# Kernel tuning notes

Hardware: AMD Instinct MI355X
Metric: run time of the kernel (lower is better)

The kernel has to match this reference:

```python
import jax, jax.numpy as jnp
import numpy as np

B, S, D = 2, 2048, 1024
H = 16
HEAD_DIM = 64          # matches head_dim init arg; D // H == 64
HALF_WINDOW = 32       # local_window_size // 2
SCALE = HEAD_DIM ** -0.5


def setup_inputs() -> dict:
    key = jax.random.key(0)
    ks = jax.random.split(key, 6)
    std = 1.0 / np.sqrt(D)
    return {
        "x": jax.random.normal(ks[0], (B, S, D), dtype=jnp.float32),
        "Wq": jax.random.normal(ks[1], (D, D), dtype=jnp.float32) * std,
        "Wk": jax.random.normal(ks[2], (D, D), dtype=jnp.float32) * std,
        "Wv": jax.random.normal(ks[3], (D, D), dtype=jnp.float32) * std,
        "Wo": jax.random.normal(ks[4], (D, D), dtype=jnp.float32) * std,
        "bo": jnp.zeros((D,), dtype=jnp.float32),
    }


def reference(x, Wq, Wk, Wv, Wo, bo):
    b, s, d = x.shape
    h, hd = H, d // H

    def split_heads(y):  # [b, s, d] -> [b, h, s, hd]
        return y.reshape(b, s, h, hd).transpose(0, 2, 1, 3)

    q = split_heads(x @ Wq) * SCALE
    k = split_heads(x @ Wk)
    v = split_heads(x @ Wv)

    # dense scores [b, h, s, s] (module materializes full O(S^2) matrix)
    scores = jnp.einsum("bhqd,bhkd->bhqk", q, k)

    # local window |i-j| <= HALF_WINDOW combined with causal j <= i
    i = jnp.arange(s)
    local = jnp.abs(i[:, None] - i[None, :]) <= HALF_WINDOW
    causal = i[None, :] <= i[:, None]
    mask = local & causal  # [s, s]
    scores = jnp.where(mask[None, None, :, :], scores, -jnp.inf)

    attn = jax.nn.softmax(scores, axis=-1)  # diagonal always valid -> no NaN
    out = jnp.einsum("bhqk,bhkd->bhqd", attn, v)
    out = out.transpose(0, 2, 1, 3).reshape(b, s, d)  # merge heads
    return out @ Wo + bo
```

## Files before the change

kernel.cpp:

```cpp
#include <hip/hip_runtime.h>
#include <hip/hip_bf16.h>

typedef __bf16 bf16_t;
typedef __bf16 bf16x8 __attribute__((ext_vector_type(8)));
typedef __bf16 bf16x4 __attribute__((ext_vector_type(4)));
typedef float  f32x4  __attribute__((ext_vector_type(4)));

#define B_   2
#define S_   2048
#define D_   1024
#define H_   16
#define HD_  64
#define HW   32
#define SCALE_ 0.125f

__device__ __forceinline__ void gl_lds16(const bf16_t* g, bf16_t* l) {
  __builtin_amdgcn_global_load_lds(
      (const __attribute__((address_space(1))) void*)g,
      (__attribute__((address_space(3))) void*)l, 16, 0, 0);
}

__global__ __launch_bounds__(256) void k_conv(const float* __restrict__ X,
                                              const float* __restrict__ W0,
                                              const float* __restrict__ W1,
                                              const float* __restrict__ W2,
                                              const float* __restrict__ W3,
                                              bf16_t* __restrict__ Xb,
                                              bf16_t* __restrict__ Wt) {
  __shared__ bf16_t t[64][72];
  int bid = blockIdx.x;
  int tid = threadIdx.x;
  if (bid < 2048) {
    int i = bid * 256 + tid;
    const float4 a = ((const float4*)X)[i * 2];
    const float4 b = ((const float4*)X)[i * 2 + 1];
    bf16x8 r;
    r[0] = (bf16_t)a.x; r[1] = (bf16_t)a.y; r[2] = (bf16_t)a.z; r[3] = (bf16_t)a.w;
    r[4] = (bf16_t)b.x; r[5] = (bf16_t)b.y; r[6] = (bf16_t)b.z; r[7] = (bf16_t)b.w;
    ((bf16x8*)Xb)[i] = r;
    return;
  }
  int wb = bid - 2048;
  int wsel = wb >> 8;
  const float* W = (wsel == 0) ? W0 : (wsel == 1) ? W1 : (wsel == 2) ? W2 : W3;
  bf16_t* dst = Wt + (size_t)wsel * D_ * D_;
  int tile = wb & 255;
  int k0 = (tile >> 4) * 64, n0 = (tile & 15) * 64;
  int r = tid >> 4, c4 = (tid & 15) * 4;
#pragma unroll
  for (int i = 0; i < 4; ++i) {
    int row = i * 16 + r;
    float4 v = *(const float4*)(W + (size_t)(k0 + row) * D_ + n0 + c4);
    t[row][c4 + 0] = (bf16_t)v.x;
    t[row][c4 + 1] = (bf16_t)v.y;
    t[row][c4 + 2] = (bf16_t)v.z;
    t[row][c4 + 3] = (bf16_t)v.w;
  }
  __syncthreads();
#pragma unroll
  for (int i = 0; i < 4; ++i) {
    int row = i * 16 + r;
    bf16x4 o;
    o[0] = t[c4 + 0][row];
    o[1] = t[c4 + 1][row];
    o[2] = t[c4 + 2][row];
    o[3] = t[c4 + 3][row];
    *(bf16x4*)(dst + (size_t)(n0 + row) * D_ + k0 + c4) = o;
  }
}

__global__ __launch_bounds__(256) void k_gemm_qkv(const bf16_t* __restrict__ X,
                                                  const bf16_t* __restrict__ Wt,
                                                  bf16_t* __restrict__ Q,
                                                  bf16_t* __restrict__ Kb,
                                                  bf16_t* __restrict__ V) {
  __shared__ bf16_t sA[3 * 128 * 32];
  __shared__ bf16_t sB[3 * 128 * 32];
  int bid = blockIdx.x;
  int mt = bid & 31, nt = bid >> 5;
  int wsel = nt >> 3;
  int n0 = (nt & 7) * 128, m0 = mt * 128;
  const bf16_t* Wp = Wt + (size_t)wsel * D_ * D_;
  int tid = threadIdx.x, lane = tid & 63, wave = tid >> 6;
  int wr = (wave >> 1) * 64, wc = (wave & 1) * 64;
  int r0 = wave * 32 + (lane >> 2);
  int ce = (((lane & 3) ^ ((lane >> 3) & 3))) * 8;
  const bf16_t* gA0 = X + (size_t)(m0 + r0) * D_ + ce;
  const bf16_t* gB0 = Wp + (size_t)(n0 + r0) * D_ + ce;
  int lofs = wave * 1024;
#define QSTAGE_(bi, kt) do { \
    gl_lds16(gA0 + (kt), sA + (bi) * 4096 + lofs);        \
    gl_lds16(gA0 + (kt) + (size_t)16 * D_, sA + (bi) * 4096 + lofs + 512); \
    gl_lds16(gB0 + (kt), sB + (bi) * 4096 + lofs);        \
    gl_lds16(gB0 + (kt) + (size_t)16 * D_, sB + (bi) * 4096 + lofs + 512); \
  } while (0)
  f32x4 acc[4][4] = {};
  int rl = lane & 15, hi = lane >> 4;
  int cofs = (hi ^ ((rl >> 1) & 3)) * 8;
  QSTAGE_(0, 0);
  QSTAGE_(1, 32);
  asm volatile("s_waitcnt vmcnt(4)" ::: "memory");
  __builtin_amdgcn_sched_barrier(0);
  __builtin_amdgcn_s_barrier();
  asm volatile("" ::: "memory");
  int cur = 0;
  for (int t = 0; t < 32; ++t) {
    const bf16_t* pA = sA + cur * 4096;
    const bf16_t* pB = sB + cur * 4096;
    bf16x8 af[4], bfr[4];
#pragma unroll
    for (int m = 0; m < 4; ++m)
      af[m] = *(const bf16x8*)&pA[(wr + m * 16 + rl) * 32 + cofs];
#pragma unroll
    for (int n = 0; n < 4; ++n)
      bfr[n] = *(const bf16x8*)&pB[(wc + n * 16 + rl) * 32 + cofs];
    int sb = cur + 2; if (sb >= 3) sb -= 3;
    if (t + 2 < 32) QSTAGE_(sb, (t + 2) * 32);
    __builtin_amdgcn_s_setprio(1);
#pragma unroll
    for (int m = 0; m < 4; ++m)
#pragma unroll
      for (int n = 0; n < 4; ++n)
        acc[m][n] = __builtin_amdgcn_mfma_f32_16x16x32_bf16(af[m], bfr[n], acc[m][n], 0, 0, 0);
    __builtin_amdgcn_s_setprio(0);
    if (t < 30) {
      asm volatile("s_waitcnt vmcnt(4)" ::: "memory");
    } else if (t == 30) {
      asm volatile("s_waitcnt vmcnt(0)" ::: "memory");
    }
    if (t < 31) {
      __builtin_amdgcn_sched_barrier(0);
      __builtin_amdgcn_s_barrier();
      asm volatile("" ::: "memory");
    }
    if (++cur == 3) cur = 0;
  }
#undef QSTAGE_
  if (wsel < 2) {
    float qscale = (wsel == 0) ? SCALE_ : 1.0f;
    bf16_t* Dst = wsel ? Kb : Q;
#pragma unroll
    for (int m = 0; m < 4; ++m) {
#pragma unroll
      for (int n = 0; n < 4; ++n) {
#pragma unroll
        for (int r = 0; r < 4; ++r) {
          int gm = m0 + wr + m * 16 + hi * 4 + r;
          int gn = n0 + wc + n * 16 + rl;
          int b = gm >> 11, s = gm & 2047;
          int h = gn >> 6, hd = gn & 63;
          Dst[(((size_t)(b * H_ + h)) * S_ + s) * HD_ + hd] = (bf16_t)(acc[m][n][r] * qscale);
        }
      }
    }
  } else {
    bf16_t* bounce = sA;
#pragma unroll
    for (int hh = 0; hh < 2; ++hh) {
      __syncthreads();
      if ((wave & 1) == hh) {
#pragma unroll
        for (int m = 0; m < 4; ++m)
#pragma unroll
          for (int n = 0; n < 4; ++n)
#pragma unroll
            for (int r = 0; r < 4; ++r)
              bounce[(n * 16 + rl) * 136 + wr + m * 16 + hi * 4 + r] = (bf16_t)acc[m][n][r];
      }
      __syncthreads();
#pragma unroll
      for (int ps = 0; ps < 4; ++ps) {
        int idx = ps * 256 + tid;
        int row = idx >> 4, c8 = (idx & 15) * 8;
        bf16x8 v = *(const bf16x8*)&bounce[row * 136 + c8];
        int gn = n0 + hh * 64 + row;
        int h = gn >> 6, hd = gn & 63;
        int gmS = m0 + c8;
        int b2 = gmS >> 11, s0 = gmS & 2047;
        *(bf16x8*)&V[(((size_t)(b2 * H_ + h)) * HD_ + hd) * S_ + s0] = v;
      }
    }
  }
}

__global__ __launch_bounds__(256) void k_gemm_out(const bf16_t* __restrict__ A,
                                                  const bf16_t* __restrict__ Wp,
                                                  const float* __restrict__ bo,
                                                  float* __restrict__ out) {
  __shared__ bf16_t sA[64 * 32];
  __shared__ bf16_t sB[128 * 32];
  int bid = blockIdx.x;
  int mt = bid & 63, nt = bid >> 6;
  int n0 = nt * 128, m0 = mt * 64;
  int tid = threadIdx.x, lane = tid & 63, wave = tid >> 6;
  int wc = wave * 32;
  int crow = lane >> 2, ccol = (lane & 3) * 8;
  const bf16_t* gsrc0; bf16_t* ldst0;
  const bf16_t* gsrc1; bf16_t* ldst1;
  const bf16_t* gsrc2; bf16_t* ldst2;
#pragma unroll
  for (int j = 0; j < 3; ++j) {
    int c = wave * 3 + j;
    const bf16_t* g; bf16_t* l;
    if (c < 4) {
      g = A + (size_t)(m0 + c * 16 + crow) * D_ + ccol;
      l = sA + c * 512;
    } else {
      g = Wp + (size_t)(n0 + (c - 4) * 16 + crow) * D_ + ccol;
      l = sB + (c - 4) * 512;
    }
    if (j == 0) { gsrc0 = g; ldst0 = l; }
    else if (j == 1) { gsrc1 = g; ldst1 = l; }
    else { gsrc2 = g; ldst2 = l; }
  }
  f32x4 acc[4][2] = {};
  int kq = (lane >> 4) * 8, rl = lane & 15, hi = lane >> 4;
  for (int kt = 0; kt < D_; kt += 32) {
    __syncthreads();
    gl_lds16(gsrc0 + kt, ldst0);
    gl_lds16(gsrc1 + kt, ldst1);
    gl_lds16(gsrc2 + kt, ldst2);
    __syncthreads();
    bf16x8 af[4], bfr[2];
#pragma unroll
    for (int m = 0; m < 4; ++m)
      af[m] = *(const bf16x8*)&sA[(m * 16 + rl) * 32 + kq];
#pragma unroll
    for (int n = 0; n < 2; ++n)
      bfr[n] = *(const bf16x8*)&sB[(wc + n * 16 + rl) * 32 + kq];
#pragma unroll
    for (int m = 0; m < 4; ++m)
#pragma unroll
      for (int n = 0; n < 2; ++n)
        acc[m][n] = __builtin_amdgcn_mfma_f32_16x16x32_bf16(af[m], bfr[n], acc[m][n], 0, 0, 0);
  }
#pragma unroll
  for (int m = 0; m < 4; ++m) {
#pragma unroll
    for (int n = 0; n < 2; ++n) {
#pragma unroll
      for (int r = 0; r < 4; ++r) {
        int gm = m0 + m * 16 + hi * 4 + r;
        int gn = n0 + wc + n * 16 + rl;
        out[(size_t)gm * D_ + gn] = acc[m][n][r] + bo[gn];
      }
    }
  }
}

#define QB 128
#define KW 160
#define VW 176
#define KLP 68
#define VTP 180

__global__ __launch_bounds__(256) void k_attn(const bf16_t* __restrict__ Q,
                                              const bf16_t* __restrict__ K,
                                              const bf16_t* __restrict__ Vt,
                                              bf16_t* __restrict__ O) {
  __shared__ bf16_t sK[KW][KLP];
  __shared__ bf16_t sV[HD_][VTP];
  __shared__ bf16_t sP[4][16][KLP];
  int bid = blockIdx.x;
  int qb = bid & 15, bh = bid >> 4;
  int q0 = qb * QB;
  const bf16_t* Kp = K + (size_t)bh * S_ * HD_;
  const bf16_t* Vp = Vt + (size_t)bh * HD_ * S_;
  const bf16_t* Qp = Q + (size_t)bh * S_ * HD_;
  int tid = threadIdx.x;
  int lane = tid & 63, wave = tid >> 6;
  int rl = lane & 15, hi = lane >> 4;
  int wk0b = q0 - HW;
  for (int idx = tid; idx < KW * 8; idx += 256) {
    int row = idx >> 3, c8 = (idx & 7) * 8;
    int kg = wk0b + row;
    kg = kg < 0 ? 0 : (kg > S_ - 1 ? S_ - 1 : kg);
    *(bf16x8*)&sK[row][c8] = *(const bf16x8*)(Kp + (size_t)kg * HD_ + c8);
  }
  for (int idx = tid; idx < HD_ * (VW / 8); idx += 256) {
    int row = idx / (VW / 8), c8 = (idx % (VW / 8)) * 8;
    int ks = wk0b + c8;
    ks = ks < 0 ? 0 : (ks > S_ - 8 ? S_ - 8 : ks);
    *(bf16x8*)&sV[row][c8] = *(const bf16x8*)(Vp + (size_t)row * S_ + ks);
  }
  __syncthreads();
  int b = bh >> 4, h = bh & 15;
#pragma unroll
  for (int qi = 0; qi < 2; ++qi) {
    int wko = qi * 64 + wave * 16;
    bf16x8 qf0 = *(const bf16x8*)(Qp + (size_t)(q0 + wko + rl) * HD_ + hi * 8);
    bf16x8 qf1 = *(const bf16x8*)(Qp + (size_t)(q0 + wko + rl) * HD_ + 32 + hi * 8);
    f32x4 accs[3] = {};
#pragma unroll
    for (int kb = 0; kb < 3; ++kb) {
      bf16x8 kf = *(const bf16x8*)&sK[wko + kb * 16 + rl][hi * 8];
      accs[kb] = __builtin_amdgcn_mfma_f32_16x16x32_bf16(kf, qf0, accs[kb], 0, 0, 0);
    }
#pragma unroll
    for (int kb = 0; kb < 3; ++kb) {
      bf16x8 kf = *(const bf16x8*)&sK[wko + kb * 16 + rl][32 + hi * 8];
      accs[kb] = __builtin_amdgcn_mfma_f32_16x16x32_bf16(kf, qf1, accs[kb], 0, 0, 0);
    }
    float p[3][4];
    float mx = -1e30f;
#pragma unroll
    for (int kb = 0; kb < 3; ++kb) {
#pragma unroll
      for (int r = 0; r < 4; ++r) {
        int kl = kb * 16 + hi * 4 + r;
        bool valid = (kl >= rl) && (kl <= rl + HW) && (wk0b + wko + kl >= 0);
        float s = valid ? accs[kb][r] : -1e30f;
        p[kb][r] = s;
        mx = fmaxf(mx, s);
      }
    }
    mx = fmaxf(mx, __shfl_xor(mx, 16));
    mx = fmaxf(mx, __shfl_xor(mx, 32));
    float sum = 0.f;
#pragma unroll
    for (int kb = 0; kb < 3; ++kb)
#pragma unroll
      for (int r = 0; r < 4; ++r) {
        p[kb][r] = __expf(p[kb][r] - mx);
        sum += p[kb][r];
      }
    sum += __shfl_xor(sum, 16);
    sum += __shfl_xor(sum, 32);
    float inv = 1.f / sum;
#pragma unroll
    for (int kb = 0; kb < 3; ++kb) {
      bf16x4 pv;
#pragma unroll
      for (int r = 0; r < 4; ++r) pv[r] = (bf16_t)(p[kb][r] * inv);
      *(bf16x4*)&sP[wave][rl][kb * 16 + hi * 4] = pv;
    }
    {
      bf16x4 z4;
#pragma unroll
      for (int r = 0; r < 4; ++r) z4[r] = (bf16_t)0.f;
      *(bf16x4*)&sP[wave][rl][48 + hi * 4] = z4;
    }
    f32x4 acco[4] = {};
#pragma unroll
    for (int ks = 0; ks < 2; ++ks) {
      bf16x8 aP = *(const bf16x8*)&sP[wave][rl][ks * 32 + hi * 8];
#pragma unroll
      for (int n = 0; n < 4; ++n) {
        bf16x8 bV = *(const bf16x8*)&sV[n * 16 + rl][wko + ks * 32 + hi * 8];
        acco[n] = __builtin_amdgcn_mfma_f32_16x16x32_bf16(aP, bV, acco[n], 0, 0, 0);
      }
    }
#pragma unroll
    for (int n = 0; n < 4; ++n) {
#pragma unroll
      for (int r = 0; r < 4; ++r) {
        int qgl = q0 + wko + hi * 4 + r;
        int d = n * 16 + rl;
        O[((size_t)(b * S_ + qgl)) * D_ + h * HD_ + d] = (bf16_t)acco[n][r];
      }
    }
  }
}

extern "C" void kernel_launch(void* const* d_in, const int* in_sizes, int n_in,
                              void* d_out, int out_size, void* d_ws, size_t ws_size,
                              hipStream_t stream) {
  const float* x  = (const float*)d_in[0];
  const float* Wq = (const float*)d_in[1];
  const float* Wk = (const float*)d_in[2];
  const float* Wv = (const float*)d_in[3];
  const float* Wo = (const float*)d_in[4];
  const float* bo = (const float*)d_in[5];
  float* out = (float*)d_out;
  char* ws = (char*)d_ws;
  bf16_t* xb = (bf16_t*)(ws);
  bf16_t* wt = (bf16_t*)(ws + (size_t)(8 << 20));
  bf16_t* qb = (bf16_t*)(ws + (size_t)(16 << 20));
  bf16_t* kb = (bf16_t*)(ws + (size_t)(24 << 20));
  bf16_t* vb = (bf16_t*)(ws + (size_t)(32 << 20));
  bf16_t* ob = (bf16_t*)(ws + (size_t)(40 << 20));

  hipLaunchKernelGGL(k_conv, dim3(3072), dim3(256), 0, stream,
                     x, Wq, Wk, Wv, Wo, xb, wt);
  hipLaunchKernelGGL(k_gemm_qkv, dim3(768), dim3(256), 0, stream, xb, wt, qb, kb, vb);
  hipLaunchKernelGGL(k_attn, dim3(512), dim3(256), 0, stream, qb, kb, vb, ob);
  hipLaunchKernelGGL(k_gemm_out, dim3(512), dim3(256), 0, stream,
                     ob, wt + (size_t)3 * D_ * D_, bo, out);
}
```

Before: 79.72 us.

## Fuse activation fp32-to-bf16 conversion into QKV GEMM A-tile loading

Drops the separate pass that converted x to bf16 in a workspace buffer; the conversion kernel now only transposes and converts the weights. The QKV GEMM reads fp32 x directly, holds the tile two steps ahead in registers, converts it to bf16, and writes it to LDS in the same swizzled layout the direct global-to-LDS loads used. This removes a full write and re-read of the bf16 activation copy and shrinks the conversion launch. In exchange the GEMM fetches twice as many bytes for A, spends registers and conversion instructions per K step, and adds an LDS-store wait before each barrier.

Measured after the change: 101.5 us. 1.27x slower.

```diff
diff --git a/kernel.cpp b/kernel.cpp
--- a/kernel.cpp
+++ b/kernel.cpp
@@ -20,31 +20,18 @@
       (__attribute__((address_space(3))) void*)l, 16, 0, 0);
 }
 
-__global__ __launch_bounds__(256) void k_conv(const float* __restrict__ X,
-                                              const float* __restrict__ W0,
-                                              const float* __restrict__ W1,
-                                              const float* __restrict__ W2,
-                                              const float* __restrict__ W3,
-                                              bf16_t* __restrict__ Xb,
-                                              bf16_t* __restrict__ Wt) {
+__global__ __launch_bounds__(256) void k_convw(const float* __restrict__ W0,
+                                               const float* __restrict__ W1,
+                                               const float* __restrict__ W2,
+                                               const float* __restrict__ W3,
+                                               bf16_t* __restrict__ Wt) {
   __shared__ bf16_t t[64][72];
   int bid = blockIdx.x;
   int tid = threadIdx.x;
-  if (bid < 2048) {
-    int i = bid * 256 + tid;
-    const float4 a = ((const float4*)X)[i * 2];
-    const float4 b = ((const float4*)X)[i * 2 + 1];
-    bf16x8 r;
-    r[0] = (bf16_t)a.x; r[1] = (bf16_t)a.y; r[2] = (bf16_t)a.z; r[3] = (bf16_t)a.w;
-    r[4] = (bf16_t)b.x; r[5] = (bf16_t)b.y; r[6] = (bf16_t)b.z; r[7] = (bf16_t)b.w;
-    ((bf16x8*)Xb)[i] = r;
-    return;
-  }
-  int wb = bid - 2048;
-  int wsel = wb >> 8;
+  int wsel = bid >> 8;
   const float* W = (wsel == 0) ? W0 : (wsel == 1) ? W1 : (wsel == 2) ? W2 : W3;
   bf16_t* dst = Wt + (size_t)wsel * D_ * D_;
-  int tile = wb & 255;
+  int tile = bid & 255;
   int k0 = (tile >> 4) * 64, n0 = (tile & 15) * 64;
   int r = tid >> 4, c4 = (tid & 15) * 4;
 #pragma unroll
@@ -69,7 +56,7 @@
   }
 }
 
-__global__ __launch_bounds__(256) void k_gemm_qkv(const bf16_t* __restrict__ X,
+__global__ __launch_bounds__(256) void k_gemm_qkv(const float* __restrict__ Xf,
                                                   const bf16_t* __restrict__ Wt,
                                                   bf16_t* __restrict__ Q,
                                                   bf16_t* __restrict__ Kb,
@@ -85,26 +72,61 @@
   int wr = (wave >> 1) * 64, wc = (wave & 1) * 64;
   int r0 = wave * 32 + (lane >> 2);
   int ce = (((lane & 3) ^ ((lane >> 3) & 3))) * 8;
-  const bf16_t* gA0 = X + (size_t)(m0 + r0) * D_ + ce;
-  const bf16_t* gB0 = Wp + (size_t)(n0 + r0) * D_ + ce;
+  const float*  gA0f = Xf + (size_t)(m0 + r0) * D_ + ce;
+  const bf16_t* gB0  = Wp + (size_t)(n0 + r0) * D_ + ce;
   int lofs = wave * 1024;
-#define QSTAGE_(bi, kt) do { \
-    gl_lds16(gA0 + (kt), sA + (bi) * 4096 + lofs);        \
-    gl_lds16(gA0 + (kt) + (size_t)16 * D_, sA + (bi) * 4096 + lofs + 512); \
-    gl_lds16(gB0 + (kt), sB + (bi) * 4096 + lofs);        \
-    gl_lds16(gB0 + (kt) + (size_t)16 * D_, sB + (bi) * 4096 + lofs + 512); \
-  } while (0)
+  int lane8 = lane * 8;
   f32x4 acc[4][4] = {};
   int rl = lane & 15, hi = lane >> 4;
   int cofs = (hi ^ ((rl >> 1) & 3)) * 8;
-  QSTAGE_(0, 0);
-  QSTAGE_(1, 32);
-  asm volatile("s_waitcnt vmcnt(4)" ::: "memory");
+  gl_lds16(gB0, sB + lofs);
+  gl_lds16(gB0 + (size_t)16 * D_, sB + lofs + 512);
+  {
+    float4 x0 = *(const float4*)(gA0f);
+    float4 x1 = *(const float4*)(gA0f + 4);
+    float4 x2 = *(const float4*)(gA0f + (size_t)16 * D_);
+    float4 x3 = *(const float4*)(gA0f + (size_t)16 * D_ + 4);
+    bf16x8 va, vb;
+    va[0] = (bf16_t)x0.x; va[1] = (bf16_t)x0.y; va[2] = (bf16_t)x0.z; va[3] = (bf16_t)x0.w;
+    va[4] = (bf16_t)x1.x; va[5] = (bf16_t)x1.y; va[6] = (bf16_t)x1.z; va[7] = (bf16_t)x1.w;
+    vb[0] = (bf16_t)x2.x; vb[1] = (bf16_t)x2.y; vb[2] = (bf16_t)x2.z; vb[3] = (bf16_t)x2.w;
+    vb[4] = (bf16_t)x3.x; vb[5] = (bf16_t)x3.y; vb[6] = (bf16_t)x3.z; vb[7] = (bf16_t)x3.w;
+    *(bf16x8*)(sA + lofs + lane8) = va;
+    *(bf16x8*)(sA + lofs + 512 + lane8) = vb;
+  }
+  float4 aR0 = *(const float4*)(gA0f + 32);
+  float4 aR1 = *(const float4*)(gA0f + 36);
+  float4 aR2 = *(const float4*)(gA0f + 32 + (size_t)16 * D_);
+  float4 aR3 = *(const float4*)(gA0f + 36 + (size_t)16 * D_);
+  gl_lds16(gB0 + 32, sB + 4096 + lofs);
+  gl_lds16(gB0 + 32 + (size_t)16 * D_, sB + 4096 + lofs + 512);
+  asm volatile("s_waitcnt vmcnt(6)" ::: "memory");
+  asm volatile("s_waitcnt lgkmcnt(0)" ::: "memory");
   __builtin_amdgcn_sched_barrier(0);
   __builtin_amdgcn_s_barrier();
   asm volatile("" ::: "memory");
   int cur = 0;
   for (int t = 0; t < 32; ++t) {
+    int wnext = cur + 1; if (wnext >= 3) wnext -= 3;
+    int sb = cur + 2; if (sb >= 3) sb -= 3;
+    if (t + 1 < 32) {
+      bf16x8 va, vb;
+      va[0] = (bf16_t)aR0.x; va[1] = (bf16_t)aR0.y; va[2] = (bf16_t)aR0.z; va[3] = (bf16_t)aR0.w;
+      va[4] = (bf16_t)aR1.x; va[5] = (bf16_t)aR1.y; va[6] = (bf16_t)aR1.z; va[7] = (bf16_t)aR1.w;
+      vb[0] = (bf16_t)aR2.x; vb[1] = (bf16_t)aR2.y; vb[2] = (bf16_t)aR2.z; vb[3] = (bf16_t)aR2.w;
+      vb[4] = (bf16_t)aR3.x; vb[5] = (bf16_t)aR3.y; vb[6] = (bf16_t)aR3.z; vb[7] = (bf16_t)aR3.w;
+      *(bf16x8*)(sA + wnext * 4096 + lofs + lane8) = va;
+      *(bf16x8*)(sA + wnext * 4096 + lofs + 512 + lane8) = vb;
+    }
+    if (t + 2 < 32) {
+      int kt2 = (t + 2) * 32;
+      aR0 = *(const float4*)(gA0f + kt2);
+      aR1 = *(const float4*)(gA0f + kt2 + 4);
+      aR2 = *(const float4*)(gA0f + kt2 + (size_t)16 * D_);
+      aR3 = *(const float4*)(gA0f + kt2 + (size_t)16 * D_ + 4);
+      gl_lds16(gB0 + kt2, sB + sb * 4096 + lofs);
+      gl_lds16(gB0 + kt2 + (size_t)16 * D_, sB + sb * 4096 + lofs + 512);
+    }
     const bf16_t* pA = sA + cur * 4096;
     const bf16_t* pB = sB + cur * 4096;
     bf16x8 af[4], bfr[4];
@@ -114,8 +136,6 @@
 #pragma unroll
     for (int n = 0; n < 4; ++n)
       bfr[n] = *(const bf16x8*)&pB[(wc + n * 16 + rl) * 32 + cofs];
-    int sb = cur + 2; if (sb >= 3) sb -= 3;
-    if (t + 2 < 32) QSTAGE_(sb, (t + 2) * 32);
     __builtin_amdgcn_s_setprio(1);
 #pragma unroll
     for (int m = 0; m < 4; ++m)
@@ -123,19 +143,19 @@
       for (int n = 0; n < 4; ++n)
         acc[m][n] = __builtin_amdgcn_mfma_f32_16x16x32_bf16(af[m], bfr[n], acc[m][n], 0, 0, 0);
     __builtin_amdgcn_s_setprio(0);
-    if (t < 30) {
-      asm volatile("s_waitcnt vmcnt(4)" ::: "memory");
+    if (t <= 29) {
+      asm volatile("s_waitcnt vmcnt(6)" ::: "memory");
     } else if (t == 30) {
       asm volatile("s_waitcnt vmcnt(0)" ::: "memory");
     }
+    asm volatile("s_waitcnt lgkmcnt(0)" ::: "memory");
     if (t < 31) {
       __builtin_amdgcn_sched_barrier(0);
       __builtin_amdgcn_s_barrier();
       asm volatile("" ::: "memory");
     }
-    if (++cur == 3) cur = 0;
-  }
-#undef QSTAGE_
+    cur = wnext;
+  }
   if (wsel < 2) {
     float qscale = (wsel == 0) ? SCALE_ : 1.0f;
     bf16_t* Dst = wsel ? Kb : Q;
@@ -373,16 +393,15 @@
   const float* bo = (const float*)d_in[5];
   float* out = (float*)d_out;
   char* ws = (char*)d_ws;
-  bf16_t* xb = (bf16_t*)(ws);
   bf16_t* wt = (bf16_t*)(ws + (size_t)(8 << 20));
   bf16_t* qb = (bf16_t*)(ws + (size_t)(16 << 20));
   bf16_t* kb = (bf16_t*)(ws + (size_t)(24 << 20));
   bf16_t* vb = (bf16_t*)(ws + (size_t)(32 << 20));
   bf16_t* ob = (bf16_t*)(ws + (size_t)(40 << 20));
 
-  hipLaunchKernelGGL(k_conv, dim3(3072), dim3(256), 0, stream,
-                     x, Wq, Wk, Wv, Wo, xb, wt);
-  hipLaunchKernelGGL(k_gemm_qkv, dim3(768), dim3(256), 0, stream, xb, wt, qb, kb, vb);
+  hipLaunchKernelGGL(k_convw, dim3(1024), dim3(256), 0, stream,
+                     Wq, Wk, Wv, Wo, wt);
+  hipLaunchKernelGGL(k_gemm_qkv, dim3(768), dim3(256), 0, stream, x, wt, qb, kb, vb);
   hipLaunchKernelGGL(k_attn, dim3(512), dim3(256), 0, stream, qb, kb, vb, ob);
   hipLaunchKernelGGL(k_gemm_out, dim3(512), dim3(256), 0, stream,
                      ob, wt + (size_t)3 * D_ * D_, bo, out);
```

## Triple-buffer output-projection GEMM with async LDS loads and one barrier per step

Applied to the files above, without the earlier changes.

Converts the output projection GEMM from a single-buffered LDS loop with two barriers per k-step into a 3-stage ring buffer. Global-to-LDS loads are issued two tiles ahead and waited on with explicit vmcnt counts. MFMA sections get a raised wave priority. This is meant to hide global load latency behind MFMA work and cut barrier stalls, at the cost of three times the LDS for this kernel and fragile hand-written waitcnt logic.

Measured after the change: 76.41 us, median of 2. 4.2% less time.

```diff
diff --git a/kernel.cpp b/kernel.cpp
--- a/kernel.cpp
+++ b/kernel.cpp
@@ -187,53 +187,78 @@
                                                   const bf16_t* __restrict__ Wp,
                                                   const float* __restrict__ bo,
                                                   float* __restrict__ out) {
-  __shared__ bf16_t sA[64 * 32];
-  __shared__ bf16_t sB[128 * 32];
+  __shared__ bf16_t sA[3 * 64 * 32];
+  __shared__ bf16_t sB[3 * 128 * 32];
   int bid = blockIdx.x;
   int mt = bid & 63, nt = bid >> 6;
   int n0 = nt * 128, m0 = mt * 64;
   int tid = threadIdx.x, lane = tid & 63, wave = tid >> 6;
   int wc = wave * 32;
   int crow = lane >> 2, ccol = (lane & 3) * 8;
-  const bf16_t* gsrc0; bf16_t* ldst0;
-  const bf16_t* gsrc1; bf16_t* ldst1;
-  const bf16_t* gsrc2; bf16_t* ldst2;
+  const bf16_t* gsrc0; int isA0, co0;
+  const bf16_t* gsrc1; int isA1, co1;
+  const bf16_t* gsrc2; int isA2, co2;
 #pragma unroll
   for (int j = 0; j < 3; ++j) {
     int c = wave * 3 + j;
-    const bf16_t* g; bf16_t* l;
+    const bf16_t* g; int isA, co;
     if (c < 4) {
       g = A + (size_t)(m0 + c * 16 + crow) * D_ + ccol;
-      l = sA + c * 512;
+      isA = 1; co = c * 512;
     } else {
       g = Wp + (size_t)(n0 + (c - 4) * 16 + crow) * D_ + ccol;
-      l = sB + (c - 4) * 512;
-    }
-    if (j == 0) { gsrc0 = g; ldst0 = l; }
-    else if (j == 1) { gsrc1 = g; ldst1 = l; }
-    else { gsrc2 = g; ldst2 = l; }
-  }
+      isA = 0; co = (c - 4) * 512;
+    }
+    if (j == 0) { gsrc0 = g; isA0 = isA; co0 = co; }
+    else if (j == 1) { gsrc1 = g; isA1 = isA; co1 = co; }
+    else { gsrc2 = g; isA2 = isA; co2 = co; }
+  }
+#define OSTAGE_(bi, kt) do { \
+    gl_lds16(gsrc0 + (kt), (isA0 ? sA + (bi) * 2048 : sB + (bi) * 4096) + co0); \
+    gl_lds16(gsrc1 + (kt), (isA1 ? sA + (bi) * 2048 : sB + (bi) * 4096) + co1); \
+    gl_lds16(gsrc2 + (kt), (isA2 ? sA + (bi) * 2048 : sB + (bi) * 4096) + co2); \
+  } while (0)
   f32x4 acc[4][2] = {};
   int kq = (lane >> 4) * 8, rl = lane & 15, hi = lane >> 4;
-  for (int kt = 0; kt < D_; kt += 32) {
-    __syncthreads();
-    gl_lds16(gsrc0 + kt, ldst0);
-    gl_lds16(gsrc1 + kt, ldst1);
-    gl_lds16(gsrc2 + kt, ldst2);
-    __syncthreads();
+  OSTAGE_(0, 0);
+  OSTAGE_(1, 32);
+  asm volatile("s_waitcnt vmcnt(3)" ::: "memory");
+  __builtin_amdgcn_sched_barrier(0);
+  __builtin_amdgcn_s_barrier();
+  asm volatile("" ::: "memory");
+  int cur = 0;
+  for (int t = 0; t < 32; ++t) {
+    const bf16_t* pA = sA + cur * 2048;
+    const bf16_t* pB = sB + cur * 4096;
     bf16x8 af[4], bfr[2];
 #pragma unroll
     for (int m = 0; m < 4; ++m)
-      af[m] = *(const bf16x8*)&sA[(m * 16 + rl) * 32 + kq];
+      af[m] = *(const bf16x8*)&pA[(m * 16 + rl) * 32 + kq];
 #pragma unroll
     for (int n = 0; n < 2; ++n)
-      bfr[n] = *(const bf16x8*)&sB[(wc + n * 16 + rl) * 32 + kq];
+      bfr[n] = *(const bf16x8*)&pB[(wc + n * 16 + rl) * 32 + kq];
+    int sb = cur + 2; if (sb >= 3) sb -= 3;
+    if (t + 2 < 32) OSTAGE_(sb, (t + 2) * 32);
+    __builtin_amdgcn_s_setprio(1);
 #pragma unroll
     for (int m = 0; m < 4; ++m)
 #pragma unroll
       for (int n = 0; n < 2; ++n)
         acc[m][n] = __builtin_amdgcn_mfma_f32_16x16x32_bf16(af[m], bfr[n], acc[m][n], 0, 0, 0);
-  }
+    __builtin_amdgcn_s_setprio(0);
+    if (t < 30) {
+      asm volatile("s_waitcnt vmcnt(3)" ::: "memory");
+    } else if (t == 30) {
+      asm volatile("s_waitcnt vmcnt(0)" ::: "memory");
+    }
+    if (t < 31) {
+      __builtin_amdgcn_sched_barrier(0);
+      __builtin_amdgcn_s_barrier();
+      asm volatile("" ::: "memory");
+    }
+    if (++cur == 3) cur = 0;
+  }
+#undef OSTAGE_
 #pragma unroll
   for (int m = 0; m < 4; ++m) {
 #pragma unroll
```
